# Performance work log

Measured on AMD Instinct MI355X. Metric: run time of the kernel, lower is better.

## Reference

```python
import jax, jax.numpy as jnp
import numpy as np

B, T, D, H, DK, DV = 2, 2048, 1024, 16, 64, 64
_MASK_ADDER = -10000.0  # tf-models MaskedSoftmax convention


def setup_inputs() -> dict:
    key = jax.random.key(0)
    ks = jax.random.split(key, 8)
    s = 0.02
    return {
        "query": jax.random.normal(ks[0], (B, T, D), jnp.float32),
        "value": jax.random.normal(ks[1], (B, T, D), jnp.float32),
        "Wq": jax.random.normal(ks[2], (D, H, DK), jnp.float32) * s,
        "bq": jnp.zeros((H, DK), jnp.float32),
        "Wk": jax.random.normal(ks[3], (D, H, DK), jnp.float32) * s,
        "bk": jnp.zeros((H, DK), jnp.float32),
        "Wv": jax.random.normal(ks[4], (D, H, DV), jnp.float32) * s,
        "bv": jnp.zeros((H, DV), jnp.float32),
        "Wo": jax.random.normal(ks[5], (H, DV, D), jnp.float32) * s,
        "bo": jnp.zeros((D,), jnp.float32),
        "attention_mask": jnp.ones((B, T, T), jnp.int32),
    }


def reference(query, value, Wq, bq, Wk, bk, Wv, bv, Wo, bo, attention_mask):
    # key defaults to value (call() with key=None); training=False -> no dropout
    q = jnp.einsum("btd,dhk->bthk", query, Wq) + bq          # [B,T,H,DK]
    k = jnp.einsum("bsd,dhk->bshk", value, Wk) + bk          # [B,S,H,DK]
    v = jnp.einsum("bsd,dhk->bshk", value, Wv) + bv          # [B,S,H,DV]
    q = q * (1.0 / jnp.sqrt(jnp.asarray(DK, q.dtype)))
    scores = jnp.einsum("bthk,bshk->bhts", q, k)             # [B,H,T,S]
    # MaskedSoftmax: expand mask at axis 1, additive -10000 on masked slots
    adder = (1.0 - attention_mask.astype(scores.dtype))[:, None, :, :] * _MASK_ADDER
    probs = jax.nn.softmax(scores + adder, axis=-1)
    ctx = jnp.einsum("bhts,bshv->bthv", probs, v)            # [B,T,H,DV]
    out = jnp.einsum("bthv,hvd->btd", ctx, Wo) + bo          # [B,T,D]
    return out
```

## Files before the change

### kernel.cpp

```cpp
#include <hip/hip_runtime.h>
#include <hip/hip_bf16.h>
#include <stdint.h>

#define TSEQ 2048
#define DMODEL 1024
#define NHEAD 16
#define HDIM 64
#define MROWS 4096
#define L2E 1.44269504088896340736f

typedef unsigned short u16;
typedef unsigned int u32;
typedef __attribute__((ext_vector_type(8))) short bf16x8;
typedef __attribute__((ext_vector_type(8))) unsigned short u16x8;
typedef __attribute__((ext_vector_type(4))) unsigned short u16x4;
typedef __attribute__((ext_vector_type(4))) float f32x4;
typedef __attribute__((ext_vector_type(16))) float f32x16;
typedef __attribute__((ext_vector_type(4))) unsigned int u32x4;

__device__ inline u16 f2bf(float f) {
  __hip_bfloat16 h(f);
  return __builtin_bit_cast(u16, h);
}

__device__ inline float fexp2(float x) { float r; asm("v_exp_f32 %0, %1" : "=v"(r) : "v"(x)); return r; }

__device__ inline unsigned cvtpk_bf16(float a, float b) {
  unsigned r; asm("v_cvt_pk_bf16_f32 %0, %1, %2" : "=v"(r) : "v"(a), "v"(b)); return r;
}

__device__ inline float fmax3(float a, float b, float c) {
  float r; asm("v_max3_f32 %0, %1, %2, %3" : "=v"(r) : "v"(a), "v"(b), "v"(c)); return r;
}

__device__ inline void permswap(u32& a, u32& b) {
  asm volatile("v_permlane32_swap_b32 %0, %1" : "+v"(a), "+v"(b));
}

__device__ inline void gload16(const void* g, void* l) {
  __builtin_amdgcn_global_load_lds((const __attribute__((address_space(1))) void*)g,
                                   (__attribute__((address_space(3))) void*)l, 16, 0, 0);
}

__global__ void prep(const float* __restrict__ q, const float* __restrict__ v,
                     u16* __restrict__ qo, u16* __restrict__ vo,
                     const float* __restrict__ Wq, const float* __restrict__ Wk,
                     const float* __restrict__ Wv, const float* __restrict__ Wo,
                     u16* __restrict__ WT3, u16* __restrict__ WoT,
                     const int* __restrict__ mask, int* __restrict__ flags) {
  __shared__ float tile[32][33];
  __shared__ int sred[4];
  const int bid = blockIdx.x, tid = threadIdx.x;
  if (bid < 8192) {
    const float* in = bid < 4096 ? q : v;
    u16* out = bid < 4096 ? qo : vo;
    const int i = (bid & 4095) * 1024 + tid * 4;
    float4 x = *(const float4*)(in + i);
    u16x4 o;
    o.x = f2bf(x.x); o.y = f2bf(x.y); o.z = f2bf(x.z); o.w = f2bf(x.w);
    *(u16x4*)(out + i) = o;
  } else if (bid < 12288) {
    int t = bid - 8192;
    const int z = t >> 10; t &= 1023;
    const float* W = z == 0 ? Wq : z == 1 ? Wk : z == 2 ? Wv : Wo;
    u16* WT = z < 3 ? (WT3 + (size_t)z * 1024 * 1024) : WoT;
    const int bx = t & 31, by = t >> 5;
    const int tr = tid >> 3;
    const int tc4 = (tid & 7) * 4;
    float4 x = *(const float4*)(W + (size_t)(by * 32 + tr) * 1024 + bx * 32 + tc4);
    tile[tr][tc4 + 0] = x.x; tile[tr][tc4 + 1] = x.y;
    tile[tr][tc4 + 2] = x.z; tile[tr][tc4 + 3] = x.w;
    __syncthreads();
    u16x4 o;
    o.x = f2bf(tile[tc4 + 0][tr]); o.y = f2bf(tile[tc4 + 1][tr]);
    o.z = f2bf(tile[tc4 + 2][tr]); o.w = f2bf(tile[tc4 + 3][tr]);
    *(u16x4*)(WT + (size_t)(bx * 32 + tr) * 1024 + by * 32 + tc4) = o;
  } else {
    const int t = bid - 12288;
    const int st = t & 15, qt = (t >> 4) & 15, b = t >> 8;
    const int row = qt * 128 + (tid >> 1);
    const int col0 = st * 128 + (tid & 1) * 64;
    const int* p = mask + (size_t)b * TSEQ * TSEQ + (size_t)row * TSEQ + col0;
    int ok = 1;
    #pragma unroll
    for (int j = 0; j < 64; j += 4) {
      int4 x = *(const int4*)(p + j);
      ok &= (x.x == 1) & (x.y == 1) & (x.z == 1) & (x.w == 1);
    }
    ok = __all(ok);
    if ((tid & 63) == 0) sred[tid >> 6] = ok;
    __syncthreads();
    if (tid == 0) flags[(b * 16 + qt) * 16 + st] = sred[0] & sred[1] & sred[2] & sred[3];
  }
}

__global__ __launch_bounds__(256) void gemm_qkv(
    const u16* __restrict__ qxb, const u16* __restrict__ vxb, const u16* __restrict__ WT3,
    const float* __restrict__ bq, const float* __restrict__ bk, const float* __restrict__ bv,
    u16* __restrict__ Qb, u16* __restrict__ Kb, u16* __restrict__ VTb, float qscale) {
  __shared__ u16 As[128 * 64];
  __shared__ u16 Bs[128 * 64];
  const int tid = threadIdx.x;
  const int w = tid >> 6, lane = tid & 63;
  const int lo = lane & 15, hi = lane >> 4;
  const int bid = blockIdx.x + (blockIdx.y << 5);
  const int swz = (bid & 7) * 96 + (bid >> 3);
  const int m0 = (swz & 31) << 7, n0 = (swz >> 5) << 7;
  const int nsel = n0 >> 10;
  const u16* A = nsel == 0 ? qxb : vxb;
  const float* bias = nsel == 0 ? bq : nsel == 1 ? bk : bv;
  const float scl = nsel == 0 ? qscale : 1.0f;
  const int wm = (w >> 1) * 64, wn = (w & 1) * 64;
  f32x4 acc[4][4] = {};
  const int loff = w * 4096 + lane * 16;
  for (int kt = 0; kt < 16; ++kt) {
    #pragma unroll
    for (int i = 0; i < 4; ++i) {
      const int off = loff + i * 1024;
      const int row = off >> 7;
      const int g = ((off >> 4) & 7) ^ (row & 7);
      gload16(A + (size_t)(m0 + row) * 1024 + kt * 64 + g * 8, (char*)As + off);
      gload16(WT3 + (size_t)(n0 + row) * 1024 + kt * 64 + g * 8, (char*)Bs + off);
    }
    __syncthreads();
    #pragma unroll
    for (int kk = 0; kk < 2; ++kk) {
      bf16x8 af[4], bfr[4];
      #pragma unroll
      for (int mi = 0; mi < 4; ++mi) {
        int row = wm + mi * 16 + lo;
        af[mi] = *(const bf16x8*)(As + row * 64 + (((kk * 4 + hi) ^ (row & 7)) << 3));
      }
      #pragma unroll
      for (int ni = 0; ni < 4; ++ni) {
        int row = wn + ni * 16 + lo;
        bfr[ni] = *(const bf16x8*)(Bs + row * 64 + (((kk * 4 + hi) ^ (row & 7)) << 3));
      }
      #pragma unroll
      for (int mi = 0; mi < 4; ++mi)
        #pragma unroll
        for (int ni = 0; ni < 4; ++ni)
          acc[mi][ni] = __builtin_amdgcn_mfma_f32_16x16x32_bf16(af[mi], bfr[ni], acc[mi][ni], 0, 0, 0);
    }
    __syncthreads();
  }
  if (nsel < 2) {
    u16* dst = nsel == 0 ? Qb : Kb;
    #pragma unroll
    for (int ni = 0; ni < 4; ++ni) {
      const int col = (n0 + wn + ni * 16 + lo) & 1023;
      const float bc = bias[col];
      #pragma unroll
      for (int mi = 0; mi < 4; ++mi) {
        #pragma unroll
        for (int r = 0; r < 4; ++r) {
          const int row = m0 + wm + mi * 16 + hi * 4 + r;
          const float v = (acc[mi][ni][r] + bc) * scl;
          dst[(size_t)(((row >> 11) * NHEAD + (col >> 6)) * TSEQ + (row & 2047)) * HDIM + (col & 63)] = f2bf(v);
        }
      }
    }
  } else {
    #pragma unroll
    for (int ni = 0; ni < 4; ++ni) {
      const int col = (n0 + wn + ni * 16 + lo) & 1023;
      const float bc = bias[col];
      const int v = col & 63;
      #pragma unroll
      for (int mi = 0; mi < 4; ++mi) {
        const int rowb = m0 + wm + mi * 16 + hi * 4;
        const int bh2 = (rowb >> 11) * NHEAD + (col >> 6);
        u16x4 pk;
        #pragma unroll
        for (int r = 0; r < 4; ++r) pk[r] = f2bf(acc[mi][ni][r] + bc);
        *(u16x4*)(VTb + ((size_t)bh2 * 64 + v) * TSEQ + (rowb & 2047)) = pk;
      }
    }
  }
}

__global__ __launch_bounds__(256) void gemm_o(const u16* __restrict__ A, const u16* __restrict__ BT,
                                              const float* __restrict__ bias, float* __restrict__ C) {
  __shared__ u16 As[64 * 64];
  __shared__ u16 Bs[128 * 64];
  const int tid = threadIdx.x;
  const int w = tid >> 6, lane = tid & 63;
  const int lo = lane & 15, hi = lane >> 4;
  const int bid = blockIdx.x + (blockIdx.y << 6);
  const int swz = (bid & 7) * 64 + (bid >> 3);
  const int m0 = (swz & 63) << 6, n0 = (swz >> 6) << 7;
  const int wm = (w >> 1) * 32, wn = (w & 1) * 64;
  f32x4 acc[2][4] = {};
  for (int kt = 0; kt < 16; ++kt) {
    #pragma unroll
    for (int i = 0; i < 2; ++i) {
      const int off = tid * 16 + i * 4096;
      const int row = off >> 7;
      const int g = ((off >> 4) & 7) ^ (row & 7);
      gload16(A + (size_t)(m0 + row) * 1024 + kt * 64 + g * 8, (char*)As + off);
    }
    #pragma unroll
    for (int i = 0; i < 4; ++i) {
      const int off = tid * 16 + i * 4096;
      const int row = off >> 7;
      const int g = ((off >> 4) & 7) ^ (row & 7);
      gload16(BT + (size_t)(n0 + row) * 1024 + kt * 64 + g * 8, (char*)Bs + off);
    }
    __syncthreads();
    #pragma unroll
    for (int kk = 0; kk < 2; ++kk) {
      bf16x8 af[2], bfr[4];
      #pragma unroll
      for (int mi = 0; mi < 2; ++mi) {
        int row = wm + mi * 16 + lo;
        af[mi] = *(const bf16x8*)(As + row * 64 + (((kk * 4 + hi) ^ (row & 7)) << 3));
      }
      #pragma unroll
      for (int ni = 0; ni < 4; ++ni) {
        int row = wn + ni * 16 + lo;
        bfr[ni] = *(const bf16x8*)(Bs + row * 64 + (((kk * 4 + hi) ^ (row & 7)) << 3));
      }
      #pragma unroll
      for (int mi = 0; mi < 2; ++mi)
        #pragma unroll
        for (int ni = 0; ni < 4; ++ni)
          acc[mi][ni] = __builtin_amdgcn_mfma_f32_16x16x32_bf16(af[mi], bfr[ni], acc[mi][ni], 0, 0, 0);
    }
    __syncthreads();
  }
  #pragma unroll
  for (int ni = 0; ni < 4; ++ni) {
    const int col = n0 + wn + ni * 16 + lo;
    const float bc = bias[col];
    #pragma unroll
    for (int mi = 0; mi < 2; ++mi)
      #pragma unroll
      for (int r = 0; r < 4; ++r) {
        const int row = m0 + wm + mi * 16 + hi * 4 + r;
        C[(size_t)row * DMODEL + col] = acc[mi][ni][r] + bc;
      }
  }
}

__global__ __launch_bounds__(256) void flash(
    const u16* __restrict__ Q, const u16* __restrict__ K, const u16* __restrict__ VT,
    const int* __restrict__ mask, const int* __restrict__ flags, u16* __restrict__ ctx) {
  __shared__ u16 Ks[2][64 * 64];
  __shared__ u16 Vs[3][64 * 64];
  const int tid = threadIdx.x, w = tid >> 6, lane = tid & 63;
  const int l5 = lane & 31, hi2 = lane >> 5;
  const int bid0 = blockIdx.x + (blockIdx.y << 4);
  const int swz = (bid0 & 7) * 64 + (bid0 >> 3);
  const int qt = swz & 15, bh = swz >> 4;
  const int b = bh >> 4, h = bh & 15;
  const int tq = qt * 128 + w * 32;

  const int soff = w * 2048 + lane * 16;
  const int srow0 = w * 16 + (lane >> 3);
  const int lg0 = (((lane & 7) ^ (lane >> 3) ^ ((w * 2) & 3)) << 3);
  const int lg1 = (((lane & 7) ^ (lane >> 3) ^ ((w * 2 + 1) & 3)) << 3);

  bf16x8 qf[4];
  #pragma unroll
  for (int kc = 0; kc < 4; ++kc)
    qf[kc] = *(const bf16x8*)(Q + ((size_t)bh * TSEQ + tq + l5) * 64 + kc * 16 + hi2 * 8);

  unsigned fl = 0;
  {
    const int* fp = flags + (b * 16 + qt) * 16;
    #pragma unroll
    for (int i = 0; i < 4; ++i) {
      int4 v = *(const int4*)(fp + i * 4);
      fl |= (unsigned)((v.x & 1) | ((v.y & 1) << 1) | ((v.z & 1) << 2) | ((v.w & 1) << 3)) << (4 * i);
    }
  }

  f32x16 o0 = {}, o1 = {};
  float mrow = -1e30f, lrow = 0.f;
  bf16x8 paA[4], paB[4];

#define STAGE_K(buf, st_) do {                                                        \
    const u16* kb_ = K + ((size_t)bh * TSEQ + (st_) * 64) * 64;                       \
    gload16(kb_ + (size_t)srow0 * 64 + lg0, (char*)Ks[buf] + soff);                   \
    gload16(kb_ + (size_t)(srow0 + 8) * 64 + lg1, (char*)Ks[buf] + soff + 1024);      \
  } while (0)
#define STAGE_V(buf, st_) do {                                                        \
    const u16* vb_ = VT + (size_t)bh * 64 * TSEQ + (st_) * 64;                        \
    gload16(vb_ + (size_t)srow0 * TSEQ + lg0, (char*)Vs[buf] + soff);                 \
    gload16(vb_ + (size_t)(srow0 + 8) * TSEQ + lg1, (char*)Vs[buf] + soff + 1024);    \
  } while (0)

#define FR(base, row, sg) \
  (*(const bf16x8*)((base) + (row) * 64 + ((((sg) ^ ((row) & 7) ^ (((row) >> 3) & 3)) << 3))))

#define QKC(T, S0, S1) do {                                                           \
    const u16* Kb_ = Ks[(T) & 1];                                                     \
    _Pragma("unroll") for (int kc = 0; kc < 4; ++kc) {                                \
      const int sg = kc * 2 + hi2;                                                    \
      S0 = __builtin_amdgcn_mfma_f32_32x32x16_bf16(FR(Kb_, l5, sg), qf[kc], S0, 0, 0, 0); \
      S1 = __builtin_amdgcn_mfma_f32_32x32x16_bf16(FR(Kb_, 32 + l5, sg), qf[kc], S1, 0, 0, 0); \
    } } while (0)

#define PVC(VB, PA) do {                                                              \
    const u16* Vb_ = Vs[VB];                                                          \
    _Pragma("unroll") for (int kc = 0; kc < 4; ++kc) {                                \
      const int sg = kc * 2 + hi2;                                                    \
      o0 = __builtin_amdgcn_mfma_f32_32x32x16_bf16(PA[kc], FR(Vb_, l5, sg), o0, 0, 0, 0); \
      o1 = __builtin_amdgcn_mfma_f32_32x32x16_bf16(PA[kc], FR(Vb_, 32 + l5, sg), o1, 0, 0, 0); \
    } } while (0)

#define SMAX(T, S0, S1, PAOUT) do {                                                   \
    if (!((fl >> ((T) >> 1)) & 1)) {                                                  \
      const int t_ = tq + l5;                                                         \
      const int* mp_ = mask + ((size_t)b * TSEQ + t_) * TSEQ + (T) * 64;              \
      _Pragma("unroll") for (int r = 0; r < 16; ++r) {                                \
        const int sr_ = (r & 3) + 8 * (r >> 2) + 4 * hi2;                             \
        S0[r] += (1.0f - (float)mp_[sr_]) * -14426.950408f;                           \
        S1[r] += (1.0f - (float)mp_[sr_ + 32]) * -14426.950408f;                      \
      } }                                                                             \
    float c0 = fmaxf(S0[0], S1[0]), c1 = fmaxf(S0[1], S1[1]);                         \
    float c2 = fmaxf(S0[2], S1[2]), c3 = fmaxf(S0[3], S1[3]);                         \
    _Pragma("unroll") for (int r = 4; r < 16; r += 4) {                               \
      c0 = fmax3(c0, S0[r], S1[r]);     c1 = fmax3(c1, S0[r+1], S1[r+1]);             \
      c2 = fmax3(c2, S0[r+2], S1[r+2]); c3 = fmax3(c3, S0[r+3], S1[r+3]); }           \
    float pm = fmax3(fmaxf(c0, c1), c2, c3);                                          \
    pm = fmaxf(pm, __shfl_xor(pm, 32));                                               \
    if (__any(pm - mrow > 11.0f)) {                                                   \
      const float mn_ = fmaxf(mrow, pm);                                              \
      const float a_ = fexp2(mrow - mn_);                                             \
      lrow *= a_; mrow = mn_;                                                         \
      _Pragma("unroll") for (int r = 0; r < 16; ++r) {                                \
        const float ar_ = __shfl(a_, (r & 3) + 8 * (r >> 2) + 4 * hi2);               \
        o0[r] *= ar_; o1[r] *= ar_; } }                                               \
    float rs = 0.f; u32 W0_[8], W1_[8];                                               \
    _Pragma("unroll") for (int q_ = 0; q_ < 4; ++q_)                                  \
      _Pragma("unroll") for (int c_ = 0; c_ < 2; ++c_) {                              \
        const int r = 4 * q_ + 2 * c_;                                                \
        float a0 = fexp2(S0[r] - mrow), b0 = fexp2(S0[r + 1] - mrow);                 \
        float a1 = fexp2(S1[r] - mrow), b1 = fexp2(S1[r + 1] - mrow);                 \
        rs += (a0 + b0) + (a1 + b1);                                                  \
        W0_[q_ * 2 + c_] = cvtpk_bf16(a0, b0);                                        \
        W1_[q_ * 2 + c_] = cvtpk_bf16(a1, b1); }                                      \
    rs += __shfl_xor(rs, 32); lrow += rs;                                             \
    _Pragma("unroll") for (int ts = 0; ts < 2; ++ts)                                  \
      _Pragma("unroll") for (int qp = 0; qp < 2; ++qp) {                              \
        u32 d0 = ts ? W1_[(2 * qp) * 2 + 0] : W0_[(2 * qp) * 2 + 0];                  \
        u32 e0 = ts ? W1_[(2 * qp + 1) * 2 + 0] : W0_[(2 * qp + 1) * 2 + 0];          \
        u32 d1 = ts ? W1_[(2 * qp) * 2 + 1] : W0_[(2 * qp) * 2 + 1];                  \
        u32 e1 = ts ? W1_[(2 * qp + 1) * 2 + 1] : W0_[(2 * qp + 1) * 2 + 1];          \
        permswap(d0, e0); permswap(d1, e1);                                           \
        u32x4 fw_; fw_.x = d0; fw_.y = d1; fw_.z = e0; fw_.w = e1;                    \
        PAOUT[ts * 2 + qp] = __builtin_bit_cast(bf16x8, fw_); }                       \
  } while (0)

#define BODY(T, VPREV, VNEXT, DOSTAGE, PAIN, PAOUT) do {                              \
    if (DOSTAGE) { STAGE_K(((T) + 1) & 1, (T) + 1); STAGE_V(VNEXT, (T) + 1); }        \
    f32x16 s0 = {}, s1 = {};                                                          \
    __builtin_amdgcn_s_setprio(1);                                                    \
    QKC(T, s0, s1);                                                                   \
    PVC(VPREV, PAIN);                                                                 \
    __builtin_amdgcn_s_setprio(0);                                                    \
    SMAX(T, s0, s1, PAOUT);                                                           \
    __syncthreads();                                                                  \
  } while (0)

  STAGE_K(0, 0); STAGE_V(0, 0);
  __syncthreads();
  {
    f32x16 s0 = {}, s1 = {};
    __builtin_amdgcn_s_setprio(1);
    QKC(0, s0, s1);
    __builtin_amdgcn_s_setprio(0);
    STAGE_K(1, 1); STAGE_V(1, 1);
    SMAX(0, s0, s1, paA);
    __syncthreads();
  }

  int vp = 0, vn = 2;
  for (int t = 1; t < 31; t += 2) {
    BODY(t, vp, vn, 1, paA, paB);
    const int vp2 = (vp + 1 == 3) ? 0 : vp + 1;
    const int vn2 = (vn + 1 == 3) ? 0 : vn + 1;
    BODY(t + 1, vp2, vn2, 1, paB, paA);
    vp = (vp2 + 1 == 3) ? 0 : vp2 + 1;
    vn = (vn2 + 1 == 3) ? 0 : vn2 + 1;
  }
  BODY(31, vp, 0, 0, paA, paB);

  __builtin_amdgcn_s_setprio(1);
  PVC(1, paB);
  __builtin_amdgcn_s_setprio(0);

#undef BODY
#undef SMAX
#undef PVC
#undef QKC
#undef FR
#undef STAGE_V
#undef STAGE_K

  const float inv = 1.0f / lrow;
  #pragma unroll
  for (int r = 0; r < 16; ++r) {
    const int sr = (r & 3) + 8 * (r >> 2) + 4 * hi2;
    const float ir = __shfl(inv, sr);
    u16* cp = ctx + (size_t)(b * TSEQ + tq + sr) * DMODEL + h * 64;
    cp[l5] = f2bf(o0[r] * ir);
    cp[32 + l5] = f2bf(o1[r] * ir);
  }
}

extern "C" void kernel_launch(void* const* d_in, const int* in_sizes, int n_in,
                              void* d_out, int out_size, void* d_ws, size_t ws_size,
                              hipStream_t stream) {
  (void)in_sizes; (void)n_in; (void)out_size; (void)ws_size;
  const float* query = (const float*)d_in[0];
  const float* value = (const float*)d_in[1];
  const float* Wq = (const float*)d_in[2];
  const float* bq = (const float*)d_in[3];
  const float* Wk = (const float*)d_in[4];
  const float* bk = (const float*)d_in[5];
  const float* Wv = (const float*)d_in[6];
  const float* bv = (const float*)d_in[7];
  const float* Wo = (const float*)d_in[8];
  const float* bo = (const float*)d_in[9];
  const int* amask = (const int*)d_in[10];

  char* ws = (char*)d_ws;
  const size_t MB = 1 << 20;
  u16* qxb = (u16*)(ws + 0 * MB);
  u16* vxb = (u16*)(ws + 8 * MB);
  u16* WT3 = (u16*)(ws + 16 * MB);
  u16* WoT = (u16*)(ws + 22 * MB);
  u16* Qb  = (u16*)(ws + 24 * MB);
  u16* Kb  = (u16*)(ws + 32 * MB);
  u16* VTb = (u16*)(ws + 48 * MB);
  u16* ctx = (u16*)(ws + 56 * MB);
  int* flg = (int*)(ws + 64 * MB);

  prep<<<12800, 256, 0, stream>>>(query, value, qxb, vxb, Wq, Wk, Wv, Wo, WT3, WoT, amask, flg);
  gemm_qkv<<<dim3(32, 24), 256, 0, stream>>>(qxb, vxb, WT3, bq, bk, bv, Qb, Kb, VTb, 0.125f * L2E);
  flash<<<dim3(16, 32), 256, 0, stream>>>(Qb, Kb, VTb, amask, flg, ctx);
  gemm_o<<<dim3(64, 8), 256, 0, stream>>>(ctx, WoT, bo, (float*)d_out);
}
```

Baseline: 144.0 us.

## Split flash attention KV range three ways and add combine kernel

The flash kernel now splits the 32 key tiles into three chunks across a third grid dimension. Each block writes unnormalised bf16 partial outputs plus row max and sum, and a new combine kernel merges them with a log-sum-exp rescale. This triples the block count from 512 to 1536 to fill more CUs and adds launch bounds for three blocks per CU, at the cost of an extra kernel launch, partial-result traffic and bf16 rounding of partials. Separately, the V-transpose epilogue in gemm_qkv now stages through swizzled shared memory so global stores are 16-byte coalesced instead of scattered 8-byte writes.

```diff
diff --git a/kernel.cpp b/kernel.cpp
--- a/kernel.cpp
+++ b/kernel.cpp
@@ -21,6 +21,9 @@
 __device__ inline u16 f2bf(float f) {
   __hip_bfloat16 h(f);
   return __builtin_bit_cast(u16, h);
+}
+__device__ inline float bf2f(u16 x) {
+  return __builtin_bit_cast(float, ((unsigned)x) << 16);
 }
 
 __device__ inline float fexp2(float x) { float r; asm("v_exp_f32 %0, %1" : "=v"(r) : "v"(x)); return r; }
@@ -98,8 +101,9 @@
     const u16* __restrict__ qxb, const u16* __restrict__ vxb, const u16* __restrict__ WT3,
     const float* __restrict__ bq, const float* __restrict__ bk, const float* __restrict__ bv,
     u16* __restrict__ Qb, u16* __restrict__ Kb, u16* __restrict__ VTb, float qscale) {
-  __shared__ u16 As[128 * 64];
-  __shared__ u16 Bs[128 * 64];
+  __shared__ u16 SMEM[2 * 128 * 64];
+  u16* As = SMEM;
+  u16* Bs = SMEM + 128 * 64;
   const int tid = threadIdx.x;
   const int w = tid >> 6, lane = tid & 63;
   const int lo = lane & 15, hi = lane >> 4;
@@ -161,20 +165,31 @@
       }
     }
   } else {
+    u16* T = SMEM;
     #pragma unroll
     for (int ni = 0; ni < 4; ++ni) {
-      const int col = (n0 + wn + ni * 16 + lo) & 1023;
-      const float bc = bias[col];
-      const int v = col & 63;
+      const int nl = wn + ni * 16 + lo;
+      const float bc = bias[(n0 + nl) & 1023];
       #pragma unroll
       for (int mi = 0; mi < 4; ++mi) {
-        const int rowb = m0 + wm + mi * 16 + hi * 4;
-        const int bh2 = (rowb >> 11) * NHEAD + (col >> 6);
+        const int mloc = wm + mi * 16 + hi * 4;
         u16x4 pk;
         #pragma unroll
         for (int r = 0; r < 4; ++r) pk[r] = f2bf(acc[mi][ni][r] + bc);
-        *(u16x4*)(VTb + ((size_t)bh2 * 64 + v) * TSEQ + (rowb & 2047)) = pk;
-      }
+        const int cg = mloc >> 3, sub = mloc & 7;
+        *(u16x4*)(T + nl * 128 + (((cg ^ (nl & 15)) << 3) + sub)) = pk;
+      }
+    }
+    __syncthreads();
+    const int b_ = m0 >> 11, t0_ = m0 & 2047;
+    #pragma unroll
+    for (int p = 0; p < 8; ++p) {
+      const int nl = p * 16 + (tid >> 4);
+      const int cg = tid & 15;
+      u16x8 val = *(const u16x8*)(T + nl * 128 + ((cg ^ (nl & 15)) << 3));
+      const int colg = (n0 + nl) & 1023;
+      u16* dst = VTb + ((size_t)(b_ * NHEAD + (colg >> 6)) * 64 + (colg & 63)) * TSEQ + t0_ + cg * 8;
+      *(u16x8*)dst = val;
     }
   }
 }
@@ -242,9 +257,10 @@
   }
 }
 
-__global__ __launch_bounds__(256) void flash(
+__global__ __launch_bounds__(256, 3) void flash3(
     const u16* __restrict__ Q, const u16* __restrict__ K, const u16* __restrict__ VT,
-    const int* __restrict__ mask, const int* __restrict__ flags, u16* __restrict__ ctx) {
+    const int* __restrict__ mask, const int* __restrict__ flags,
+    u16* __restrict__ Op, float2* __restrict__ ml) {
   __shared__ u16 Ks[2][64 * 64];
   __shared__ u16 Vs[3][64 * 64];
   const int tid = threadIdx.x, w = tid >> 6, lane = tid & 63;
@@ -252,7 +268,10 @@
   const int bid0 = blockIdx.x + (blockIdx.y << 4);
   const int swz = (bid0 & 7) * 64 + (bid0 >> 3);
   const int qt = swz & 15, bh = swz >> 4;
-  const int b = bh >> 4, h = bh & 15;
+  const int kvh = blockIdx.z;
+  const int NT = (kvh == 2) ? 10 : 11;
+  const int st0 = kvh * 11;
+  const int b = bh >> 4;
   const int tq = qt * 128 + w * 32;
 
   const int soff = w * 2048 + lane * 16;
@@ -293,8 +312,8 @@
 #define FR(base, row, sg) \
   (*(const bf16x8*)((base) + (row) * 64 + ((((sg) ^ ((row) & 7) ^ (((row) >> 3) & 3)) << 3))))
 
-#define QKC(T, S0, S1) do {                                                           \
-    const u16* Kb_ = Ks[(T) & 1];                                                     \
+#define QKC(KB, S0, S1) do {                                                          \
+    const u16* Kb_ = Ks[KB];                                                          \
     _Pragma("unroll") for (int kc = 0; kc < 4; ++kc) {                                \
       const int sg = kc * 2 + hi2;                                                    \
       S0 = __builtin_amdgcn_mfma_f32_32x32x16_bf16(FR(Kb_, l5, sg), qf[kc], S0, 0, 0, 0); \
@@ -309,10 +328,10 @@
       o1 = __builtin_amdgcn_mfma_f32_32x32x16_bf16(PA[kc], FR(Vb_, 32 + l5, sg), o1, 0, 0, 0); \
     } } while (0)
 
-#define SMAX(T, S0, S1, PAOUT) do {                                                   \
-    if (!((fl >> ((T) >> 1)) & 1)) {                                                  \
+#define SMAX(TG, S0, S1, PAOUT) do {                                                  \
+    if (!((fl >> ((TG) >> 1)) & 1)) {                                                 \
       const int t_ = tq + l5;                                                         \
-      const int* mp_ = mask + ((size_t)b * TSEQ + t_) * TSEQ + (T) * 64;              \
+      const int* mp_ = mask + ((size_t)b * TSEQ + t_) * TSEQ + (TG) * 64;             \
       _Pragma("unroll") for (int r = 0; r < 16; ++r) {                                \
         const int sr_ = (r & 3) + 8 * (r >> 2) + 4 * hi2;                             \
         S0[r] += (1.0f - (float)mp_[sr_]) * -14426.950408f;                           \
@@ -353,43 +372,50 @@
         PAOUT[ts * 2 + qp] = __builtin_bit_cast(bf16x8, fw_); }                       \
   } while (0)
 
-#define BODY(T, VPREV, VNEXT, DOSTAGE, PAIN, PAOUT) do {                              \
-    if (DOSTAGE) { STAGE_K(((T) + 1) & 1, (T) + 1); STAGE_V(VNEXT, (T) + 1); }        \
+#define BODY(IT, VPREV, VNEXT, DOSTAGE, PAIN, PAOUT) do {                             \
+    if (DOSTAGE) { STAGE_K(((IT) + 1) & 1, st0 + (IT) + 1); STAGE_V(VNEXT, st0 + (IT) + 1); } \
     f32x16 s0 = {}, s1 = {};                                                          \
     __builtin_amdgcn_s_setprio(1);                                                    \
-    QKC(T, s0, s1);                                                                   \
+    QKC((IT) & 1, s0, s1);                                                            \
     PVC(VPREV, PAIN);                                                                 \
     __builtin_amdgcn_s_setprio(0);                                                    \
-    SMAX(T, s0, s1, PAOUT);                                                           \
+    SMAX(st0 + (IT), s0, s1, PAOUT);                                                  \
     __syncthreads();                                                                  \
   } while (0)
 
-  STAGE_K(0, 0); STAGE_V(0, 0);
+  STAGE_K(0, st0); STAGE_V(0, st0);
   __syncthreads();
   {
     f32x16 s0 = {}, s1 = {};
     __builtin_amdgcn_s_setprio(1);
     QKC(0, s0, s1);
     __builtin_amdgcn_s_setprio(0);
-    STAGE_K(1, 1); STAGE_V(1, 1);
-    SMAX(0, s0, s1, paA);
+    STAGE_K(1, st0 + 1); STAGE_V(1, st0 + 1);
+    SMAX(st0, s0, s1, paA);
     __syncthreads();
   }
 
   int vp = 0, vn = 2;
-  for (int t = 1; t < 31; t += 2) {
-    BODY(t, vp, vn, 1, paA, paB);
+  int it = 1;
+  for (; it + 1 < NT; it += 2) {
+    BODY(it, vp, vn, 1, paA, paB);
     const int vp2 = (vp + 1 == 3) ? 0 : vp + 1;
     const int vn2 = (vn + 1 == 3) ? 0 : vn + 1;
-    BODY(t + 1, vp2, vn2, 1, paB, paA);
+    BODY(it + 1, vp2, vn2, (it + 2 < NT), paB, paA);
     vp = (vp2 + 1 == 3) ? 0 : vp2 + 1;
     vn = (vn2 + 1 == 3) ? 0 : vn2 + 1;
   }
-  BODY(31, vp, 0, 0, paA, paB);
-
-  __builtin_amdgcn_s_setprio(1);
-  PVC(1, paB);
-  __builtin_amdgcn_s_setprio(0);
+  if ((NT & 1) == 0) {
+    BODY(NT - 1, vp, vn, 0, paA, paB);
+    vp = (vp + 1 == 3) ? 0 : vp + 1;
+    __builtin_amdgcn_s_setprio(1);
+    PVC(vp, paB);
+    __builtin_amdgcn_s_setprio(0);
+  } else {
+    __builtin_amdgcn_s_setprio(1);
+    PVC(vp, paA);
+    __builtin_amdgcn_s_setprio(0);
+  }
 
 #undef BODY
 #undef SMAX
@@ -399,15 +425,41 @@
 #undef STAGE_V
 #undef STAGE_K
 
-  const float inv = 1.0f / lrow;
+  const size_t rbase = (size_t)kvh * 65536 + (size_t)bh * TSEQ;
+  if (hi2 == 0)
+    ml[rbase + tq + l5] = make_float2(mrow, lrow);
   #pragma unroll
   for (int r = 0; r < 16; ++r) {
     const int sr = (r & 3) + 8 * (r >> 2) + 4 * hi2;
-    const float ir = __shfl(inv, sr);
-    u16* cp = ctx + (size_t)(b * TSEQ + tq + sr) * DMODEL + h * 64;
-    cp[l5] = f2bf(o0[r] * ir);
-    cp[32 + l5] = f2bf(o1[r] * ir);
-  }
+    u16* cp = Op + (rbase + tq + sr) * 64;
+    cp[l5] = f2bf(o0[r]);
+    cp[32 + l5] = f2bf(o1[r]);
+  }
+}
+
+__global__ __launch_bounds__(256) void combine3(const u16* __restrict__ Op,
+                                                const float2* __restrict__ ml,
+                                                u16* __restrict__ ctx) {
+  const int tid = threadIdx.x;
+  const int row = blockIdx.x * 16 + (tid >> 4);
+  const int c4 = (tid & 15) * 4;
+  const float2 A = ml[row];
+  const float2 B = ml[65536 + row];
+  const float2 Cm = ml[131072 + row];
+  const float m = fmax3(A.x, B.x, Cm.x);
+  float eA = fexp2(A.x - m), eB = fexp2(B.x - m), eC = fexp2(Cm.x - m);
+  const float inv = 1.0f / (A.y * eA + B.y * eB + Cm.y * eC);
+  eA *= inv; eB *= inv; eC *= inv;
+  u16x4 oa = *(const u16x4*)(Op + (size_t)row * 64 + c4);
+  u16x4 ob = *(const u16x4*)(Op + ((size_t)65536 + row) * 64 + c4);
+  u16x4 oc = *(const u16x4*)(Op + ((size_t)131072 + row) * 64 + c4);
+  float v0 = bf2f(oa.x) * eA + bf2f(ob.x) * eB + bf2f(oc.x) * eC;
+  float v1 = bf2f(oa.y) * eA + bf2f(ob.y) * eB + bf2f(oc.y) * eC;
+  float v2 = bf2f(oa.z) * eA + bf2f(ob.z) * eB + bf2f(oc.z) * eC;
+  float v3 = bf2f(oa.w) * eA + bf2f(ob.w) * eB + bf2f(oc.w) * eC;
+  uint2 pw = make_uint2(cvtpk_bf16(v0, v1), cvtpk_bf16(v2, v3));
+  const int b = row >> 15, h = (row >> 11) & 15, t = row & 2047;
+  *(uint2*)(ctx + ((size_t)(b * TSEQ + t)) * DMODEL + h * 64 + c4) = pw;
 }
 
 extern "C" void kernel_launch(void* const* d_in, const int* in_sizes, int n_in,
@@ -431,15 +483,18 @@
   u16* qxb = (u16*)(ws + 0 * MB);
   u16* vxb = (u16*)(ws + 8 * MB);
   u16* WT3 = (u16*)(ws + 16 * MB);
-  u16* WoT = (u16*)(ws + 22 * MB);
   u16* Qb  = (u16*)(ws + 24 * MB);
   u16* Kb  = (u16*)(ws + 32 * MB);
+  float2* ml = (float2*)(ws + 40 * MB);
+  int* flg = (int*)(ws + 42 * MB);
+  u16* WoT = (u16*)(ws + 44 * MB);
   u16* VTb = (u16*)(ws + 48 * MB);
   u16* ctx = (u16*)(ws + 56 * MB);
-  int* flg = (int*)(ws + 64 * MB);
+  u16* Op  = (u16*)(ws + 0 * MB);
 
   prep<<<12800, 256, 0, stream>>>(query, value, qxb, vxb, Wq, Wk, Wv, Wo, WT3, WoT, amask, flg);
   gemm_qkv<<<dim3(32, 24), 256, 0, stream>>>(qxb, vxb, WT3, bq, bk, bv, Qb, Kb, VTb, 0.125f * L2E);
-  flash<<<dim3(16, 32), 256, 0, stream>>>(Qb, Kb, VTb, amask, flg, ctx);
+  flash3<<<dim3(16, 32, 3), 256, 0, stream>>>(Qb, Kb, VTb, amask, flg, Op, ml);
+  combine3<<<4096, 256, 0, stream>>>(Op, ml, ctx);
   gemm_o<<<dim3(64, 8), 256, 0, stream>>>(ctx, WoT, bo, (float*)d_out);
 }
```

New measurement: 150.6 us. +4.6%, slower.
